# Performance work log

Measured on AMD Instinct MI355X. Metric: run time of the kernel, lower is better.

Reference implementation:

```python
import jax, jax.numpy as jnp
import numpy as np

HEADS = 8
KEY_DIM = 64
GROUPS = 16
EPS = 1e-5


def setup_inputs() -> dict:
    key = jax.random.key(0)
    ks = jax.random.split(key, 7)
    b, c, h, w = 4, 256, 128, 128
    dk = KEY_DIM * HEADS  # 512
    x = jax.random.normal(ks[0], (b, c, h, w), dtype=jnp.float32)
    wq = jax.random.normal(ks[1], (dk, c), dtype=jnp.float32) * 0.02      # to_q (1x1, no bias)
    wkv = jax.random.normal(ks[2], (2 * dk, c), dtype=jnp.float32) * 0.02  # to_kv (1x1, no bias)
    wo = jax.random.normal(ks[3], (c, dk), dtype=jnp.float32) * 0.02       # to_out weight (1x1)
    bo = jax.random.normal(ks[4], (c,), dtype=jnp.float32) * 0.02          # to_out bias
    gamma = jnp.ones((2 * c,), dtype=jnp.float32)                          # GroupNorm weight
    beta = jnp.zeros((2 * c,), dtype=jnp.float32)                          # GroupNorm bias
    return {"x": x, "wq": wq, "wkv": wkv, "wo": wo, "bo": bo, "gamma": gamma, "beta": beta}


def reference(x, wq, wkv, wo, bo, gamma, beta):
    b, c, h, w = x.shape
    n = h * w
    xf = x.reshape(b, c, n)

    # 1x1 conv projections == channel GEMMs
    q = jnp.einsum('dc,bcn->bdn', wq, xf).reshape(b, HEADS, KEY_DIM, n)
    kv = jnp.einsum('dc,bcn->bdn', wkv, xf)
    k, v = jnp.split(kv, 2, axis=1)
    k = k.reshape(b, HEADS, KEY_DIM, n)
    v = v.reshape(b, HEADS, KEY_DIM, n)

    scale = KEY_DIM ** (-0.25)
    k = jax.nn.softmax(k * scale, axis=-1)   # softmax over spatial n
    q = jax.nn.softmax(q * scale, axis=-2)   # norm_queries: softmax over key_dim

    ctx = jnp.einsum('bhdn,bhen->bhde', k, v)   # [b,h,64,64]
    out = jnp.einsum('bhdn,bhde->bhen', q, ctx)  # [b,h,64,n]
    out = out.reshape(b, HEADS * KEY_DIM, n)

    out = jnp.einsum('od,bdn->bon', wo, out) + bo[None, :, None]  # to_out 1x1 conv

    y = jnp.concatenate([out, xf], axis=1)  # [b, 2c, n]
    c2 = 2 * c
    yg = y.reshape(b, GROUPS, (c2 // GROUPS) * n)
    mean = yg.mean(axis=2, keepdims=True)
    var = yg.var(axis=2, keepdims=True)
    yn = ((yg - mean) * jax.lax.rsqrt(var + EPS)).reshape(b, c2, n)
    yn = yn * gamma[None, :, None] + beta[None, :, None]
    return yn.reshape(b, c2, h, w)
```

## Files before the change

kernel.cpp:

```cpp
#include <hip/hip_runtime.h>

typedef int    i32x4 __attribute__((ext_vector_type(4)));
typedef float  f32x4 __attribute__((ext_vector_type(4)));
typedef __bf16 bf16x8 __attribute__((ext_vector_type(8)));
union B16 { i32x4 i; bf16x8 v; };

#define NN 16384
#define QSCALE 0.35355339059327373f
#define EPSV 1e-5f
#define GRPN 524288.0f

#define GSUM_OFF 0
#define GSQ_OFF  64
#define WS_ZERO_FLOATS 128


__device__ __forceinline__ ushort f2bfu(float f) {
  union { __bf16 h; ushort u; } c; c.h = (__bf16)f; return c.u;
}
__device__ __forceinline__ uint packbf2(float lo, float hi) {
  return (uint)f2bfu(lo) | ((uint)f2bfu(hi) << 16);
}
__device__ __forceinline__ void gload_lds16(const void* g, void* l) {
  __builtin_amdgcn_global_load_lds(
      (const __attribute__((address_space(1))) void*)g,
      (__attribute__((address_space(3))) void*)l, 16, 0, 0);
}

__global__ __launch_bounds__(256) void k_cvt(const float* __restrict__ s,
                                             ushort* __restrict__ d, int n) {
  int i = (blockIdx.x * 256 + threadIdx.x) * 4;
  if (i >= n) return;
  float4 v = *(const float4*)(s + i);
  uint2 p; p.x = packbf2(v.x, v.y); p.y = packbf2(v.z, v.w);
  *(uint2*)(d + i) = p;
}

__global__ __launch_bounds__(256) void k0_xprep(const float* __restrict__ x,
                                                float* __restrict__ outp,
                                                float* ws) {
  const int t = threadIdx.x;
  const int n0 = blockIdx.x * 64, cg = blockIdx.y, b = blockIdx.z;
  __shared__ __align__(16) uint tile[64 * 17];
  const int c = t >> 3;
  const int nb = (t & 7) * 8;
  const float* src = x + ((size_t)(b * 256 + cg * 32 + c)) * NN + n0 + nb;
  float v[8];
  { float4 a0 = *(const float4*)src; float4 a1 = *(const float4*)(src + 4);
    v[0]=a0.x; v[1]=a0.y; v[2]=a0.z; v[3]=a0.w; v[4]=a1.x; v[5]=a1.y; v[6]=a1.z; v[7]=a1.w; }
  float s = 0.f, s2 = 0.f;
  #pragma unroll
  for (int j = 0; j < 8; ++j) { s += v[j]; s2 += v[j] * v[j]; }
  float th[8];
  #pragma unroll
  for (int j = 0; j < 8; ++j) th[j] = __shfl_xor(v[j], 8);
  const bool even = ((t >> 3) & 1) == 0;
  const int cp = t >> 4;
  #pragma unroll
  for (int jj = 0; jj < 4; ++jj) {
    const int j = even ? jj : (4 + jj);
    const float lo = even ? v[j] : th[j];
    const float hi = even ? th[j] : v[j];
    tile[(nb + j) * 17 + cp] = packbf2(lo, hi);
  }
  __syncthreads();
  {
    const int n = t >> 2, co = (t & 3) * 4;
    uint o0 = tile[n*17+co], o1 = tile[n*17+co+1], o2 = tile[n*17+co+2], o3 = tile[n*17+co+3];
    ushort* xT = (ushort*)(outp + ((size_t)(b * 512 + 256)) * NN);
    ushort* dst = xT + (size_t)(n0 + n) * 256 + cg * 32 + (t & 3) * 8;
    i32x4 pk; pk[0] = (int)o0; pk[1] = (int)o1; pk[2] = (int)o2; pk[3] = (int)o3;
    *(i32x4*)dst = pk;
  }
  #pragma unroll
  for (int m = 1; m <= 32; m <<= 1) { s += __shfl_xor(s, m); s2 += __shfl_xor(s2, m); }
  __shared__ float rs[4], rq[4];
  const int w = t >> 6;
  if ((t & 63) == 0) { rs[w] = s; rq[w] = s2; }
  __syncthreads();
  if (t == 0) {
    atomicAdd(&ws[GSUM_OFF + b * 16 + 8 + cg], rs[0] + rs[1] + rs[2] + rs[3]);
    atomicAdd(&ws[GSQ_OFF  + b * 16 + 8 + cg], rq[0] + rq[1] + rq[2] + rq[3]);
  }
}

__global__ __launch_bounds__(512)
__attribute__((amdgpu_waves_per_eu(2, 2)))
void k1_kvctx(const float* outp,
              const ushort* __restrict__ wkv_bf,
              float* __restrict__ ctxpA,
              float* __restrict__ ctxpB,
              float* __restrict__ ksump) {
  const int t = threadIdx.x, lane = t & 63, w = t >> 6;
  const int l15 = lane & 15, l4 = lane >> 4;
  const int chunk = blockIdx.x, hq = blockIdx.y, b = blockIdx.z;
  const ushort* xT = (const ushort*)(outp + ((size_t)(b * 512 + 256)) * NN);
  __shared__ __align__(16) ushort xt[2][16384];
  __shared__ __align__(16) ushort kvb[2][8192];

  const int nbase = chunk * 512;

  auto STAGE = [&](ushort* bufp, int st) {
    #pragma unroll
    for (int j = 0; j < 4; ++j) {
      const int rl = w * 8 + j * 2 + (lane >> 5);
      const int slot = (lane & 31) ^ (rl & 31);
      const ushort* gp = xT + (size_t)(nbase + st * 64 + rl) * 256 + slot * 8;
      gload_lds16(gp, bufp + (w * 8 + j * 2) * 256);
    }
  };

  STAGE(xt[0], 0);

  const int rbase0 = (w < 4) ? (16 * w) : (512 + 16 * (w - 4));
  B16 afr[4][8];
  #pragma unroll
  for (int hi = 0; hi < 4; ++hi) {
    const int h = hq * 4 + hi;
    const ushort* wr = wkv_bf + (size_t)(rbase0 + h * 64 + l15) * 256 + l4 * 8;
    #pragma unroll
    for (int ks = 0; ks < 8; ++ks) afr[hi][ks].i = *(const i32x4*)(wr + ks * 32);
  }
  #pragma unroll
  for (int hi = 0; hi < 4; ++hi)
    #pragma unroll
    for (int ks = 0; ks < 8; ++ks)
      asm volatile("" : "+v"(afr[hi][ks].i));

  f32x4 ctxc[4][2];
  #pragma unroll
  for (int hi = 0; hi < 4; ++hi)
    #pragma unroll
    for (int ct = 0; ct < 2; ++ct) ctxc[hi][ct] = f32x4{0.f, 0.f, 0.f, 0.f};
  float ksp[4] = {0.f, 0.f, 0.f, 0.f};

  asm volatile("s_waitcnt vmcnt(0)" ::: "memory");
  __builtin_amdgcn_s_barrier();

  const int kvrow = ((w < 4) ? 16 * w : 64 + 16 * (w - 4)) + l15;

  for (int st = 0; st < 8; ++st) {
    const int cur = st & 1;
    if (st < 7) {
      STAGE(xt[cur ^ 1], st + 1);
      asm volatile("s_waitcnt vmcnt(4)" ::: "memory");
    } else {
      asm volatile("s_waitcnt vmcnt(0)" ::: "memory");
    }
    __builtin_amdgcn_s_barrier();
    const ushort* xb = xt[cur];

    #pragma unroll
    for (int hp2 = 0; hp2 < 2; ++hp2) {
      f32x4 acc[2][4];
      #pragma unroll
      for (int hi2 = 0; hi2 < 2; ++hi2)
        #pragma unroll
        for (int ct = 0; ct < 4; ++ct) acc[hi2][ct] = f32x4{0.f, 0.f, 0.f, 0.f};
      #pragma unroll
      for (int ks = 0; ks < 8; ++ks) {
        B16 bfr[4];
        #pragma unroll
        for (int ct = 0; ct < 4; ++ct) {
          const int n = ct * 16 + l15;
          const int slot = (ks * 4 + l4) ^ (n & 31);
          bfr[ct].i = *(const i32x4*)((const char*)xb + n * 512 + slot * 16);
        }
        #pragma unroll
        for (int hi2 = 0; hi2 < 2; ++hi2)
          #pragma unroll
          for (int ct = 0; ct < 4; ++ct)
            acc[hi2][ct] = __builtin_amdgcn_mfma_f32_16x16x32_bf16(
                bfr[ct].v, afr[hp2 * 2 + hi2][ks].v, acc[hi2][ct], 0, 0, 0);
      }
      #pragma unroll
      for (int hi2 = 0; hi2 < 2; ++hi2) {
        char* kb = (char*)kvb[hi2];
        #pragma unroll
        for (int ct = 0; ct < 4; ++ct) {
          float v0 = acc[hi2][ct][0], v1 = acc[hi2][ct][1];
          float v2 = acc[hi2][ct][2], v3 = acc[hi2][ct][3];
          if (w < 4) {
            v0 = __expf(v0 * QSCALE); v1 = __expf(v1 * QSCALE);
            v2 = __expf(v2 * QSCALE); v3 = __expf(v3 * QSCALE);
            ksp[hp2 * 2 + hi2] += (v0 + v1) + (v2 + v3);
          }
          uint2 pk; pk.x = packbf2(v0, v1); pk.y = packbf2(v2, v3);
          const int nn0 = ct * 16 + l4 * 4;
          *(uint2*)(kb + kvrow * 128 + (((nn0 >> 3) ^ (kvrow & 7)) << 4) + (nn0 & 7) * 2) = pk;
        }
      }
      asm volatile("s_waitcnt lgkmcnt(0)" ::: "memory");
      __builtin_amdgcn_s_barrier();
      #pragma unroll
      for (int hi2 = 0; hi2 < 2; ++hi2) {
        const char* kb = (const char*)kvb[hi2];
        #pragma unroll
        for (int ks = 0; ks < 2; ++ks) {
          const int ar = 16 * (w & 3) + l15;
          B16 a;
          a.i = *(const i32x4*)(kb + ar * 128 + (((ks * 4 + l4) ^ (ar & 7)) << 4));
          #pragma unroll
          for (int ct = 0; ct < 2; ++ct) {
            const int br = 64 + (w >> 2) * 32 + ct * 16 + l15;
            B16 bb;
            bb.i = *(const i32x4*)(kb + br * 128 + (((ks * 4 + l4) ^ (br & 7)) << 4));
            ctxc[hp2 * 2 + hi2][ct] = __builtin_amdgcn_mfma_f32_16x16x32_bf16(
                a.v, bb.v, ctxc[hp2 * 2 + hi2][ct], 0, 0, 0);
          }
        }
      }
      asm volatile("s_waitcnt lgkmcnt(0)" ::: "memory");
      __builtin_amdgcn_s_barrier();
    }
  }

  if (w < 4) {
    #pragma unroll
    for (int hi = 0; hi < 4; ++hi) {
      float s = ksp[hi];
      s += __shfl_xor(s, 16);
      s += __shfl_xor(s, 32);
      if (lane < 16)
        ksump[chunk * 2048 + (b * 8 + hq * 4 + hi) * 64 + 16 * w + l15] = s;
    }
  }
  float* base = (chunk < 16 ? ctxpA : ctxpB) + (size_t)(chunk & 15) * 131072;
  #pragma unroll
  for (int hi = 0; hi < 4; ++hi) {
    float* cp = base + (size_t)(b * 8 + hq * 4 + hi) * 4096;
    #pragma unroll
    for (int ct = 0; ct < 2; ++ct)
      #pragma unroll
      for (int r = 0; r < 4; ++r)
        cp[(16 * (w & 3) + l4 * 4 + r) * 64 + (w >> 2) * 32 + ct * 16 + l15] = ctxc[hi][ct][r];
  }
}

__global__ __launch_bounds__(256) void k1b_weff(const float* __restrict__ ctxpA,
                                                const float* __restrict__ ctxpB,
                                                const float* __restrict__ ksump,
                                                const ushort* __restrict__ wo_bf,
                                                ushort* __restrict__ weff_bf) {
  const int t = threadIdx.x, lane = t & 63, w = t >> 6;
  const int l15 = lane & 15, l4 = lane >> 4;
  const int h = blockIdx.x, b = blockIdx.y;
  __shared__ float ksinv[64];
  __shared__ __align__(16) float ctxs[64 * 68];
  if (t < 64) {
    float s = 0.f;
    #pragma unroll
    for (int c = 0; c < 32; ++c) s += ksump[c * 2048 + (b * 8 + h) * 64 + t];
    ksinv[t] = 1.f / s;
  }
  const int off = (b * 8 + h) * 4096;
  for (int i = t; i < 4096; i += 256) {
    float s = 0.f;
    #pragma unroll
    for (int c = 0; c < 16; ++c) s += ctxpA[(size_t)c * 131072 + off + i];
    #pragma unroll
    for (int c = 0; c < 16; ++c) s += ctxpB[(size_t)c * 131072 + off + i];
    ctxs[(i >> 6) * 68 + (i & 63)] = s;
  }
  __syncthreads();
  f32x4 acc[4][4];
  #pragma unroll
  for (int m = 0; m < 4; ++m)
    #pragma unroll
    for (int ct = 0; ct < 4; ++ct) acc[m][ct] = f32x4{0.f, 0.f, 0.f, 0.f};
  #pragma unroll
  for (int ks = 0; ks < 2; ++ks) {
    B16 bfr[4];
    #pragma unroll
    for (int ct = 0; ct < 4; ++ct) {
      const int d = ct * 16 + l15;
      const float inv = ksinv[d];
      const float* bp = &ctxs[d * 68 + ks * 32 + l4 * 8];
      #pragma unroll
      for (int j = 0; j < 4; ++j) {
        bfr[ct].v[j] = (__bf16)(bp[j] * inv);
        bfr[ct].v[4 + j] = (__bf16)(bp[4 + j] * inv);
      }
    }
    #pragma unroll
    for (int m = 0; m < 4; ++m) {
      B16 af;
      af.i = *(const i32x4*)(wo_bf + (size_t)(w * 64 + m * 16 + l15) * 512 + h * 64 + ks * 32 + l4 * 8);
      #pragma unroll
      for (int ct = 0; ct < 4; ++ct)
        acc[m][ct] = __builtin_amdgcn_mfma_f32_16x16x32_bf16(af.v, bfr[ct].v, acc[m][ct], 0, 0, 0);
    }
  }
  #pragma unroll
  for (int m = 0; m < 4; ++m)
    #pragma unroll
    for (int ct = 0; ct < 4; ++ct)
      #pragma unroll
      for (int r = 0; r < 4; ++r)
        weff_bf[((size_t)b * 256 + w * 64 + m * 16 + l4 * 4 + r) * 512 + h * 64 + ct * 16 + l15]
            = f2bfu(acc[m][ct][r]);
}

__global__ __launch_bounds__(256, 2) void k2_qy(float* outp,
                                                const ushort* __restrict__ wq_bf,
                                                const ushort* __restrict__ weff_bf,
                                                const float* __restrict__ bo,
                                                float* ws) {
  const int t = threadIdx.x, lane = t & 63, w = t >> 6;
  const int l15 = lane & 15, l4 = lane >> 4;
  const int n0 = blockIdx.x * 64, b = blockIdx.y;
  const ushort* xT = (const ushort*)(outp + ((size_t)(b * 512 + 256)) * NN);
  __shared__ __align__(16) ushort xt[64 * 256];
  __shared__ __align__(16) ushort PT[64 * 256];
  __shared__ float rsum[4][2], rsq[4][2];
  {
    const int n = t >> 2;
    const ushort* srcp = xT + (size_t)(n0 + n) * 256 + (t & 3) * 64;
    #pragma unroll
    for (int i = 0; i < 8; ++i) {
      const int slot = ((t & 3) * 8 + i) ^ (n & 31);
      *(i32x4*)((char*)xt + n * 512 + slot * 16) = *(const i32x4*)(srcp + i * 8);
    }
  }
  __syncthreads();
  f32x4 yacc[4][4];
  #pragma unroll
  for (int m = 0; m < 4; ++m)
    #pragma unroll
    for (int ct = 0; ct < 4; ++ct) yacc[m][ct] = f32x4{0.f, 0.f, 0.f, 0.f};

  for (int hp = 0; hp < 2; ++hp) {
    const int h = hp * 4 + w;
    f32x4 qacc[4][4];
    #pragma unroll
    for (int mt = 0; mt < 4; ++mt)
      #pragma unroll
      for (int ct = 0; ct < 4; ++ct) qacc[mt][ct] = f32x4{0.f, 0.f, 0.f, 0.f};
    #pragma unroll 2
    for (int ks = 0; ks < 8; ++ks) {
      B16 bfr[4];
      #pragma unroll
      for (int ct = 0; ct < 4; ++ct) {
        const int n = ct * 16 + l15;
        const int slot = (ks * 4 + l4) ^ (n & 31);
        bfr[ct].i = *(const i32x4*)((const char*)xt + n * 512 + slot * 16);
      }
      #pragma unroll
      for (int mt = 0; mt < 4; ++mt) {
        B16 af;
        af.i = *(const i32x4*)(wq_bf + (size_t)(h * 64 + mt * 16 + l15) * 256 + ks * 32 + l4 * 8);
        #pragma unroll
        for (int ct = 0; ct < 4; ++ct)
          qacc[mt][ct] = __builtin_amdgcn_mfma_f32_16x16x32_bf16(af.v, bfr[ct].v, qacc[mt][ct], 0, 0, 0);
      }
    }
    #pragma unroll
    for (int ct = 0; ct < 4; ++ct) {
      float sv[4][4]; float mx = -1e30f;
      #pragma unroll
      for (int mt = 0; mt < 4; ++mt)
        #pragma unroll
        for (int r = 0; r < 4; ++r) {
          sv[mt][r] = qacc[mt][ct][r] * QSCALE;
          mx = fmaxf(mx, sv[mt][r]);
        }
      mx = fmaxf(mx, __shfl_xor(mx, 16)); mx = fmaxf(mx, __shfl_xor(mx, 32));
      float ssum = 0.f;
      #pragma unroll
      for (int mt = 0; mt < 4; ++mt)
        #pragma unroll
        for (int r = 0; r < 4; ++r) { sv[mt][r] = __expf(sv[mt][r] - mx); ssum += sv[mt][r]; }
      ssum += __shfl_xor(ssum, 16); ssum += __shfl_xor(ssum, 32);
      const float inv = 1.f / ssum;
      const int n = ct * 16 + l15;
      #pragma unroll
      for (int mt = 0; mt < 4; ++mt)
        #pragma unroll
        for (int rp = 0; rp < 2; ++rp) {
          const uint pk = packbf2(sv[mt][2 * rp] * inv, sv[mt][2 * rp + 1] * inv);
          const int hd = w * 64 + mt * 16 + l4 * 4 + 2 * rp;
          *(uint*)((char*)PT + ((n * 512 + hd * 2) ^ ((n & 31) << 4))) = pk;
        }
    }
    __syncthreads();
    #pragma unroll 2
    for (int ks = 0; ks < 8; ++ks) {
      B16 bfr[4];
      #pragma unroll
      for (int ct = 0; ct < 4; ++ct) {
        const int n = ct * 16 + l15;
        const int slot = (ks * 4 + l4) ^ (n & 31);
        bfr[ct].i = *(const i32x4*)((const char*)PT + n * 512 + slot * 16);
      }
      #pragma unroll
      for (int m = 0; m < 4; ++m) {
        B16 af;
        af.i = *(const i32x4*)(weff_bf + ((size_t)b * 256 + w * 64 + m * 16 + l15) * 512
                               + hp * 256 + ks * 32 + l4 * 8);
        #pragma unroll
        for (int ct = 0; ct < 4; ++ct)
          yacc[m][ct] = __builtin_amdgcn_mfma_f32_16x16x32_bf16(af.v, bfr[ct].v, yacc[m][ct], 0, 0, 0);
      }
    }
    __syncthreads();
  }
  float sg[2] = {0.f, 0.f}, qg[2] = {0.f, 0.f};
  #pragma unroll
  for (int m = 0; m < 4; ++m) {
    const int o = w * 64 + m * 16 + l4 * 4;
    const f32x4 bv = *(const f32x4*)(bo + o);
    const int gi = m >> 1;
    #pragma unroll
    for (int ct = 0; ct < 4; ++ct)
      #pragma unroll
      for (int r = 0; r < 4; ++r) {
        const float val = yacc[m][ct][r] + bv[r];
        yacc[m][ct][r] = val;
        sg[gi] += val; qg[gi] += val * val;
      }
  }
  #pragma unroll
  for (int msk = 1; msk <= 32; msk <<= 1) {
    sg[0] += __shfl_xor(sg[0], msk); sg[1] += __shfl_xor(sg[1], msk);
    qg[0] += __shfl_xor(qg[0], msk); qg[1] += __shfl_xor(qg[1], msk);
  }
  if (lane == 0) { rsum[w][0] = sg[0]; rsum[w][1] = sg[1]; rsq[w][0] = qg[0]; rsq[w][1] = qg[1]; }
  __syncthreads();
  if (t < 8) {
    atomicAdd(&ws[GSUM_OFF + b * 16 + t], rsum[t >> 1][t & 1]);
    atomicAdd(&ws[GSQ_OFF + b * 16 + t], rsq[t >> 1][t & 1]);
  }
  #pragma unroll
  for (int m = 0; m < 4; ++m)
    #pragma unroll
    for (int ct = 0; ct < 4; ++ct)
      #pragma unroll
      for (int r = 0; r < 4; ++r)
        outp[((size_t)(b * 512) + w * 64 + m * 16 + l4 * 4 + r) * NN + n0 + ct * 16 + l15]
            = yacc[m][ct][r];
}

__global__ __launch_bounds__(256) void k3_groupnorm(
    const float* __restrict__ x, const float* __restrict__ gamma,
    const float* __restrict__ beta, const float* __restrict__ ws,
    float* out) {
  const int t = threadIdx.x;
  const int b = blockIdx.z, ch = blockIdx.y;
  const int n0 = blockIdx.x * 1024 + t * 4;
  const int g = ch >> 5;
  const float s = ws[GSUM_OFF + b * 16 + g];
  const float s2 = ws[GSQ_OFF + b * 16 + g];
  const float mean = s / GRPN;
  const float var = s2 / GRPN - mean * mean;
  const float inv = rsqrtf(var + EPSV);
  const float ga = gamma[ch] * inv;
  const float be = beta[ch] - mean * ga;
  float* op = out + ((size_t)(b * 512) + ch) * NN + n0;
  float4 v;
  if (ch < 256) v = *(const float4*)op;
  else v = *(const float4*)(x + ((size_t)(b * 256) + (ch - 256)) * NN + n0);
  v.x = v.x * ga + be;
  v.y = v.y * ga + be;
  v.z = v.z * ga + be;
  v.w = v.w * ga + be;
  *(float4*)op = v;
}

extern "C" void kernel_launch(void* const* d_in, const int* in_sizes, int n_in,
                              void* d_out, int out_size, void* d_ws, size_t ws_size,
                              hipStream_t stream) {
  const float* x     = (const float*)d_in[0];
  const float* wq    = (const float*)d_in[1];
  const float* wkv   = (const float*)d_in[2];
  const float* wo    = (const float*)d_in[3];
  const float* bo    = (const float*)d_in[4];
  const float* gamma = (const float*)d_in[5];
  const float* beta  = (const float*)d_in[6];
  float* out = (float*)d_out;
  float* ws = (float*)d_ws;

  float* spare0 = out + (size_t)256 * NN;
  ushort* wq_bf   = (ushort*)(spare0 + 2097152);
  ushort* wkv_bf  = wq_bf + 131072;
  ushort* wo_bf   = wkv_bf + 262144;
  ushort* weff_bf = wo_bf + 131072;
  float*  ksump   = (float*)(weff_bf + 524288);
  float*  ctxpA   = out + (size_t)(2 * 512 + 256) * NN + 2097152;
  float*  ctxpB   = out + (size_t)(3 * 512 + 256) * NN + 2097152;

  hipMemsetAsync(ws, 0, WS_ZERO_FLOATS * sizeof(float), stream);
  k_cvt<<<128, 256, 0, stream>>>(wq,  wq_bf,  131072);
  k_cvt<<<256, 256, 0, stream>>>(wkv, wkv_bf, 262144);
  k_cvt<<<128, 256, 0, stream>>>(wo,  wo_bf,  131072);
  k0_xprep<<<dim3(256, 8, 4), 256, 0, stream>>>(x, out, ws);
  k1_kvctx<<<dim3(32, 2, 4), 512, 0, stream>>>(out, wkv_bf, ctxpA, ctxpB, ksump);
  k1b_weff<<<dim3(8, 4), 256, 0, stream>>>(ctxpA, ctxpB, ksump, wo_bf, weff_bf);
  k2_qy<<<dim3(256, 4), 256, 0, stream>>>(out, wq_bf, weff_bf, bo, ws);
  k3_groupnorm<<<dim3(16, 512, 4), 256, 0, stream>>>(x, gamma, beta, ws, out);
}
```

Baseline: 287.7 us.

## Merge weight conversions, widen xprep blocks, and use direct-to-LDS loads in k2

The three bf16 weight-conversion launches become one kernel that picks its source array by index, which relies on wq_bf, wkv_bf and wo_bf sitting contiguously. k0_xprep now has each block handle all 8 channel groups for a 64-column strip, writing full 512-byte rows of the transposed x, issuing fewer atomics and launching far fewer blocks. The cost is more registers and a larger LDS tile per block. k2_qy stages x through global_load_lds with an XOR swizzle instead of register round-trips, saving VGPRs and instructions.

```diff
diff --git a/kernel.cpp b/kernel.cpp
--- a/kernel.cpp
+++ b/kernel.cpp
@@ -27,11 +27,16 @@
       (__attribute__((address_space(3))) void*)l, 16, 0, 0);
 }
 
-__global__ __launch_bounds__(256) void k_cvt(const float* __restrict__ s,
-                                             ushort* __restrict__ d, int n) {
+__global__ __launch_bounds__(256) void k_cvt3(const float* __restrict__ a,
+                                              const float* __restrict__ bsrc,
+                                              const float* __restrict__ c,
+                                              ushort* __restrict__ d) {
   int i = (blockIdx.x * 256 + threadIdx.x) * 4;
-  if (i >= n) return;
-  float4 v = *(const float4*)(s + i);
+  const float* s; int off;
+  if (i < 131072)      { s = a;    off = 0; }
+  else if (i < 393216) { s = bsrc; off = 131072; }
+  else                 { s = c;    off = 393216; }
+  float4 v = *(const float4*)(s + (i - off));
   uint2 p; p.x = packbf2(v.x, v.y); p.y = packbf2(v.z, v.w);
   *(uint2*)(d + i) = p;
 }
@@ -40,47 +45,70 @@
                                                 float* __restrict__ outp,
                                                 float* ws) {
   const int t = threadIdx.x;
-  const int n0 = blockIdx.x * 64, cg = blockIdx.y, b = blockIdx.z;
-  __shared__ __align__(16) uint tile[64 * 17];
-  const int c = t >> 3;
+  const int n0 = blockIdx.x * 64, b = blockIdx.z;
+  __shared__ __align__(16) uint tile[64 * 130];
+  const int cl = t >> 3;
   const int nb = (t & 7) * 8;
-  const float* src = x + ((size_t)(b * 256 + cg * 32 + c)) * NN + n0 + nb;
-  float v[8];
-  { float4 a0 = *(const float4*)src; float4 a1 = *(const float4*)(src + 4);
-    v[0]=a0.x; v[1]=a0.y; v[2]=a0.z; v[3]=a0.w; v[4]=a1.x; v[5]=a1.y; v[6]=a1.z; v[7]=a1.w; }
-  float s = 0.f, s2 = 0.f;
-  #pragma unroll
-  for (int j = 0; j < 8; ++j) { s += v[j]; s2 += v[j] * v[j]; }
-  float th[8];
-  #pragma unroll
-  for (int j = 0; j < 8; ++j) th[j] = __shfl_xor(v[j], 8);
   const bool even = ((t >> 3) & 1) == 0;
-  const int cp = t >> 4;
-  #pragma unroll
-  for (int jj = 0; jj < 4; ++jj) {
-    const int j = even ? jj : (4 + jj);
-    const float lo = even ? v[j] : th[j];
-    const float hi = even ? th[j] : v[j];
-    tile[(nb + j) * 17 + cp] = packbf2(lo, hi);
+  const int cpl = t >> 4;
+
+  float4 va[8][2];
+  #pragma unroll
+  for (int cg = 0; cg < 8; ++cg) {
+    const float* src = x + ((size_t)(b * 256 + cg * 32 + cl)) * NN + n0 + nb;
+    va[cg][0] = *(const float4*)src;
+    va[cg][1] = *(const float4*)(src + 4);
+  }
+
+  float s[8], s2[8];
+  #pragma unroll
+  for (int g = 0; g < 8; ++g) { s[g] = 0.f; s2[g] = 0.f; }
+
+  #pragma unroll
+  for (int cg = 0; cg < 8; ++cg) {
+    float v[8] = {va[cg][0].x, va[cg][0].y, va[cg][0].z, va[cg][0].w,
+                  va[cg][1].x, va[cg][1].y, va[cg][1].z, va[cg][1].w};
+    #pragma unroll
+    for (int j = 0; j < 8; ++j) { s[cg] += v[j]; s2[cg] += v[j] * v[j]; }
+    float th[8];
+    #pragma unroll
+    for (int j = 0; j < 8; ++j) th[j] = __shfl_xor(v[j], 8);
+    const int col = cg * 16 + cpl;
+    #pragma unroll
+    for (int jj = 0; jj < 4; ++jj) {
+      const int j = even ? jj : (4 + jj);
+      const float lo = even ? v[j] : th[j];
+      const float hi = even ? th[j] : v[j];
+      tile[(nb + j) * 130 + col] = packbf2(lo, hi);
+    }
   }
   __syncthreads();
   {
-    const int n = t >> 2, co = (t & 3) * 4;
-    uint o0 = tile[n*17+co], o1 = tile[n*17+co+1], o2 = tile[n*17+co+2], o3 = tile[n*17+co+3];
     ushort* xT = (ushort*)(outp + ((size_t)(b * 512 + 256)) * NN);
-    ushort* dst = xT + (size_t)(n0 + n) * 256 + cg * 32 + (t & 3) * 8;
-    i32x4 pk; pk[0] = (int)o0; pk[1] = (int)o1; pk[2] = (int)o2; pk[3] = (int)o3;
-    *(i32x4*)dst = pk;
-  }
-  #pragma unroll
-  for (int m = 1; m <= 32; m <<= 1) { s += __shfl_xor(s, m); s2 += __shfl_xor(s2, m); }
-  __shared__ float rs[4], rq[4];
+    const int slot = t & 31;
+    #pragma unroll
+    for (int p = 0; p < 8; ++p) {
+      const int n = p * 8 + (t >> 5);
+      const uint* tp = &tile[n * 130 + slot * 4];
+      i32x4 pk; pk[0] = (int)tp[0]; pk[1] = (int)tp[1]; pk[2] = (int)tp[2]; pk[3] = (int)tp[3];
+      *(i32x4*)(xT + (size_t)(n0 + n) * 256 + slot * 8) = pk;
+    }
+  }
+  #pragma unroll
+  for (int g = 0; g < 8; ++g)
+    #pragma unroll
+    for (int m = 1; m <= 32; m <<= 1) {
+      s[g] += __shfl_xor(s[g], m); s2[g] += __shfl_xor(s2[g], m);
+    }
+  __shared__ float rs[4][8], rq[4][8];
   const int w = t >> 6;
-  if ((t & 63) == 0) { rs[w] = s; rq[w] = s2; }
+  if ((t & 63) == 0)
+    #pragma unroll
+    for (int g = 0; g < 8; ++g) { rs[w][g] = s[g]; rq[w][g] = s2[g]; }
   __syncthreads();
-  if (t == 0) {
-    atomicAdd(&ws[GSUM_OFF + b * 16 + 8 + cg], rs[0] + rs[1] + rs[2] + rs[3]);
-    atomicAdd(&ws[GSQ_OFF  + b * 16 + 8 + cg], rq[0] + rq[1] + rq[2] + rq[3]);
+  if (t < 8) {
+    atomicAdd(&ws[GSUM_OFF + b * 16 + 8 + t], rs[0][t] + rs[1][t] + rs[2][t] + rs[3][t]);
+    atomicAdd(&ws[GSQ_OFF  + b * 16 + 8 + t], rq[0][t] + rq[1][t] + rq[2][t] + rq[3][t]);
   }
 }
 
@@ -314,15 +342,16 @@
   __shared__ __align__(16) ushort PT[64 * 256];
   __shared__ float rsum[4][2], rsq[4][2];
   {
-    const int n = t >> 2;
-    const ushort* srcp = xT + (size_t)(n0 + n) * 256 + (t & 3) * 64;
-    #pragma unroll
-    for (int i = 0; i < 8; ++i) {
-      const int slot = ((t & 3) * 8 + i) ^ (n & 31);
-      *(i32x4*)((char*)xt + n * 512 + slot * 16) = *(const i32x4*)(srcp + i * 8);
-    }
-  }
-  __syncthreads();
+    #pragma unroll
+    for (int j = 0; j < 8; ++j) {
+      const int rl = w * 16 + j * 2 + (lane >> 5);
+      const int slot = (lane & 31) ^ (rl & 31);
+      const ushort* gp = xT + (size_t)(n0 + rl) * 256 + slot * 8;
+      gload_lds16(gp, xt + (w * 16 + j * 2) * 256);
+    }
+    asm volatile("s_waitcnt vmcnt(0)" ::: "memory");
+    __builtin_amdgcn_s_barrier();
+  }
   f32x4 yacc[4][4];
   #pragma unroll
   for (int m = 0; m < 4; ++m)
@@ -489,10 +518,8 @@
   float*  ctxpB   = out + (size_t)(3 * 512 + 256) * NN + 2097152;
 
   hipMemsetAsync(ws, 0, WS_ZERO_FLOATS * sizeof(float), stream);
-  k_cvt<<<128, 256, 0, stream>>>(wq,  wq_bf,  131072);
-  k_cvt<<<256, 256, 0, stream>>>(wkv, wkv_bf, 262144);
-  k_cvt<<<128, 256, 0, stream>>>(wo,  wo_bf,  131072);
-  k0_xprep<<<dim3(256, 8, 4), 256, 0, stream>>>(x, out, ws);
+  k_cvt3<<<512, 256, 0, stream>>>(wq, wkv, wo, wq_bf);
+  k0_xprep<<<dim3(256, 1, 4), 256, 0, stream>>>(x, out, ws);
   k1_kvctx<<<dim3(32, 2, 4), 512, 0, stream>>>(out, wkv_bf, ctxpA, ctxpB, ksump);
   k1b_weff<<<dim3(8, 4), 256, 0, stream>>>(ctxpA, ctxpB, ksump, wo_bf, weff_bf);
   k2_qy<<<dim3(256, 4), 256, 0, stream>>>(out, wq_bf, weff_bf, bo, ws);
```

New measurement: 244.4 us. 15.1% less time.
